# Kernel tuning notes

Measured on AMD Instinct MI355X. Metric: run time of the kernel, lower is better.

## Reference

```python
import jax, jax.numpy as jnp
import numpy as np

S = 30.0   # scale
M = 0.3    # additive angular margin (arcface)
EPS = 1e-07


def setup_inputs() -> dict:
    key = jax.random.key(0)
    k1, k2, k3 = jax.random.split(key, 3)
    N, D, C = 8192, 256, 10000
    x = jax.random.normal(k1, (N, D), dtype=jnp.float32)
    W = jax.random.normal(k2, (C, D), dtype=jnp.float32) * 0.05  # linear weight [C, D]
    target = jax.random.randint(k3, (N,), 0, C)
    return {"x": x, "W": W, "target": target}


def reference(x, W, target):
    # L2-normalize inputs along features. NOTE: the torch code's loop that
    # 'normalizes' weight_fc params is a no-op (rebinds a local), so W is
    # intentionally NOT normalized here, matching the original math.
    xn = x / jnp.linalg.norm(x, axis=1, keepdims=True)
    logits = xn @ W.T                                   # [N, C]
    n = logits.shape[0]
    tgt = logits[jnp.arange(n), target]                 # [N] target-class cosine-like score
    # arcface margin: s * cos(acos(clamp(t)) + m)
    numerator = S * jnp.cos(jnp.arccos(jnp.clip(tgt, -1.0 + EPS, 1.0 - EPS)) + M)
    # exclude-target sum: sum_j exp(s*logits) minus the target column (no [N,C-1] concat)
    exp_s = jnp.exp(S * logits)                         # [N, C]
    sum_excl = jnp.sum(exp_s, axis=1) - jnp.exp(S * tgt)
    denominator = jnp.exp(numerator) + sum_excl
    L = numerator - jnp.log(denominator)
    return -jnp.mean(L)
```

## Files before the change

kernel.cpp:

```cpp
#include <hip/hip_runtime.h>
#include <hip/hip_bf16.h>
#include <stdint.h>

#define S_SCALE 30.0f
#define S_L2E_SC 0.33813165020835f
#define N_ROWS 8192
#define D_DIM 256
#define C_CLS 10000
#define NCB 8

typedef __attribute__((ext_vector_type(4))) float f32x4;

static __device__ __forceinline__ void gl16(const void* g, void* l) {
  __builtin_amdgcn_global_load_lds(
      (const __attribute__((address_space(1))) void*)g,
      (__attribute__((address_space(3))) void*)l, 16, 0, 0);
}

static __device__ __forceinline__ long u2l(uint2 v) {
  union { uint2 u; long l; } x; x.u = v; return x.l;
}

static __device__ __forceinline__ float row_sum16(float v) {
  union { float f; int i; } u, w;
  u.f = v;
  w.i = __builtin_amdgcn_update_dpp(0, u.i, 0xB1, 0xF, 0xF, true);  u.f += w.f;
  w.i = __builtin_amdgcn_update_dpp(0, u.i, 0x4E, 0xF, 0xF, true);  u.f += w.f;
  w.i = __builtin_amdgcn_update_dpp(0, u.i, 0x141, 0xF, 0xF, true); u.f += w.f;
  w.i = __builtin_amdgcn_update_dpp(0, u.i, 0x140, 0xF, 0xF, true); u.f += w.f;
  return u.f;
}

__global__ __launch_bounds__(256) void k_prep(const float* __restrict__ x,
                                              const float* __restrict__ W,
                                              const int* __restrict__ target,
                                              unsigned char* __restrict__ xnb8,
                                              unsigned char* __restrict__ WbF8,
                                              float* __restrict__ tgt) {
  if (blockIdx.x < 1280) {
    int gidx = blockIdx.x * 256 + threadIdx.x;
    int lane = gidx & 63;
    int kc = (gidx >> 6) & 7;
    int c16 = gidx >> 9;
    int col = c16 * 16 + (lane & 15);
    int k0 = kc * 32 + (lane >> 4) * 8;
    int r0 = 0, r1 = 0;
    if (col < C_CLS) {
      const float4 a = *(const float4*)(W + (size_t)col * D_DIM + k0);
      const float4 b = *(const float4*)(W + (size_t)col * D_DIM + k0 + 4);
      r0 = __builtin_amdgcn_cvt_pk_fp8_f32(a.x * 16.f, a.y * 16.f, 0, false);
      r0 = __builtin_amdgcn_cvt_pk_fp8_f32(a.z * 16.f, a.w * 16.f, r0, true);
      r1 = __builtin_amdgcn_cvt_pk_fp8_f32(b.x * 16.f, b.y * 16.f, 0, false);
      r1 = __builtin_amdgcn_cvt_pk_fp8_f32(b.z * 16.f, b.w * 16.f, r1, true);
    }
    *(int2*)(WbF8 + (size_t)gidx * 8) = (int2){r0, r1};
  } else {
    int row = (blockIdx.x - 1280) * 4 + (threadIdx.x >> 6);
    int l = threadIdx.x & 63;
    const float4 v = *(const float4*)(x + (size_t)row * D_DIM + l * 4);
    float ss = v.x * v.x + v.y * v.y + v.z * v.z + v.w * v.w;
#pragma unroll
    for (int m = 1; m < 64; m <<= 1) ss += __shfl_xor(ss, m, 64);
    float rn = 1.0f / sqrtf(ss);
    float s8 = rn * 8.f;
    int r0 = __builtin_amdgcn_cvt_pk_fp8_f32(v.x * s8, v.y * s8, 0, false);
    r0 = __builtin_amdgcn_cvt_pk_fp8_f32(v.z * s8, v.w * s8, r0, true);
    int j = l >> 1, e = l & 1;
    int panel = row >> 7, r16 = (row >> 4) & 7, lr = row & 15;
    size_t dst = (size_t)panel * 32768 + (size_t)(r16 * 8 + (j >> 2)) * 512 +
                 (size_t)((j & 3) * 16 + lr) * 8 + e * 4;
    *(int*)(xnb8 + dst) = r0;
    int tc = target[row];
    const float4 b = *(const float4*)(W + (size_t)tc * D_DIM + l * 4);
    float s = v.x * b.x + v.y * b.y + v.z * b.z + v.w * b.w;
#pragma unroll
    for (int m = 1; m < 64; m <<= 1) s += __shfl_xor(s, m, 64);
    if (l == 0) tgt[row] = s * rn;
  }
}

__global__ __launch_bounds__(512, 4) void k_gemm(const unsigned char* __restrict__ xnb8,
                                                 const unsigned char* __restrict__ WbF8,
                                                 float* __restrict__ partials) {
  __shared__ __align__(16) char lds[34816];
  const int b = blockIdx.x;
  const int cg = b & 7;
  const int br = b >> 3;
  const int bc0 = cg * 5;
  const int t = threadIdx.x;
  const int w = t >> 6, l = t & 63;
  const int wr = w >> 2, wc = w & 3;
  const int lr = l & 15, lk = l >> 4;
  float* rsumAll = (float*)(lds + 32768);

  if (t < 512) rsumAll[t] = 0.f;

  {
    const char* Ag = (const char*)xnb8 + (size_t)br * 32768;
#pragma unroll
    for (int i = 0; i < 4; ++i)
      gl16(Ag + i * 8192 + w * 1024 + l * 16, lds + i * 8192 + w * 1024);
    asm volatile("s_waitcnt vmcnt(0)" ::: "memory");
    __builtin_amdgcn_sched_barrier(0);
    __builtin_amdgcn_s_barrier();
  }

  f32x4 acc[4][4];
#pragma unroll
  for (int m = 0; m < 4; m++)
#pragma unroll
    for (int n = 0; n < 4; n++) acc[m][n] = (f32x4){0.f, 0.f, 0.f, 0.f};

  const char* AwL = lds + (size_t)(wr * 4 * 8) * 512 + (size_t)l * 8;
  const unsigned char* Bw = WbF8 + (size_t)(bc0 * 16 + wc * 4) * 4096 + (size_t)l * 8;
  float* rw = rsumAll + w * 64;

  uint2 b0[4], b1[4];
#pragma unroll
  for (int fn = 0; fn < 4; ++fn) b0[fn] = *(const uint2*)(Bw + fn * 4096);

  for (int tt = 0; tt < 5; ++tt) {
    auto step = [&](int kc, uint2(&cur)[4], uint2(&nxt)[4]) {
      if (kc < 7) {
#pragma unroll
        for (int fn = 0; fn < 4; ++fn)
          nxt[fn] = *(const uint2*)(Bw + fn * 4096 + (kc + 1) * 512);
      } else if (tt < 4) {
#pragma unroll
        for (int fn = 0; fn < 4; ++fn)
          nxt[fn] = *(const uint2*)(Bw + 65536 + fn * 4096);
      }
#pragma unroll
      for (int fm = 0; fm < 4; ++fm) {
        long a = u2l(*(const uint2*)(AwL + (fm * 8 + kc) * 512));
#pragma unroll
        for (int fn = 0; fn < 4; ++fn)
          acc[fm][fn] = __builtin_amdgcn_mfma_f32_16x16x32_fp8_fp8(
              a, u2l(cur[fn]), acc[fm][fn], 0, 0, 0);
      }
    };
    step(0, b0, b1); step(1, b1, b0); step(2, b0, b1); step(3, b1, b0);
    step(4, b0, b1); step(5, b1, b0); step(6, b0, b1); step(7, b1, b0);

    const int bc = bc0 + tt;
#pragma unroll
    for (int m = 0; m < 4; ++m) {
      float rs0 = 0.f, rs1 = 0.f, rs2 = 0.f, rs3 = 0.f;
#pragma unroll
      for (int n = 0; n < 4; ++n) {
        int col = bc * 256 + wc * 64 + n * 16 + lr;
        bool ok = (col < C_CLS);
        rs0 += ok ? __builtin_amdgcn_exp2f(acc[m][n][0] * S_L2E_SC) : 0.f;
        rs1 += ok ? __builtin_amdgcn_exp2f(acc[m][n][1] * S_L2E_SC) : 0.f;
        rs2 += ok ? __builtin_amdgcn_exp2f(acc[m][n][2] * S_L2E_SC) : 0.f;
        rs3 += ok ? __builtin_amdgcn_exp2f(acc[m][n][3] * S_L2E_SC) : 0.f;
        acc[m][n] = (f32x4){0.f, 0.f, 0.f, 0.f};
      }
      rs0 = row_sum16(rs0); rs1 = row_sum16(rs1);
      rs2 = row_sum16(rs2); rs3 = row_sum16(rs3);
      if (lr == 0) {
        int row = m * 16 + lk * 4;
        rw[row + 0] += rs0; rw[row + 1] += rs1;
        rw[row + 2] += rs2; rw[row + 3] += rs3;
      }
    }
    Bw += 65536;
  }

  __syncthreads();
  if (t < 128) {
    int wr2 = t >> 6, r = t & 63;
    float sv = rsumAll[(wr2 * 4 + 0) * 64 + r] + rsumAll[(wr2 * 4 + 1) * 64 + r] +
               rsumAll[(wr2 * 4 + 2) * 64 + r] + rsumAll[(wr2 * 4 + 3) * 64 + r];
    partials[(size_t)cg * N_ROWS + (size_t)br * 128 + t] = sv;
  }
}

__global__ __launch_bounds__(256) void k_loss1(const float* __restrict__ partials,
                                               const float* __restrict__ tgt,
                                               float* __restrict__ bsum) {
  __shared__ float wsum[4];
  int i = blockIdx.x * 256 + threadIdx.x;
  const float* p = partials + i;
  float s = 0.f;
#pragma unroll
  for (int j = 0; j < NCB; ++j) s += p[(size_t)j * N_ROWS];
  float tl = tgt[i];
  float tcv = fminf(fmaxf(tl, -1.0f + 1e-7f), 1.0f - 1e-7f);
  const float cm = 0.95533648912560601964f;
  const float sm = 0.29552020666133957510f;
  float num = S_SCALE * (tcv * cm - sqrtf(fmaxf(1.0f - tcv * tcv, 0.f)) * sm);
  float sum_excl = s - __expf(S_SCALE * tl);
  float denom = __expf(num) + sum_excl;
  float L = num - __logf(denom);
#pragma unroll
  for (int m = 1; m < 64; m <<= 1) L += __shfl_xor(L, m, 64);
  int l = threadIdx.x & 63, w = threadIdx.x >> 6;
  if (l == 0) wsum[w] = L;
  __syncthreads();
  if (threadIdx.x == 0) bsum[blockIdx.x] = wsum[0] + wsum[1] + wsum[2] + wsum[3];
}

__global__ void k_loss2(const float* __restrict__ bsum, float* __restrict__ out) {
  float s = 0.f;
  for (int i = 0; i < 32; ++i) s += bsum[i];
  out[0] = -s / (float)N_ROWS;
}

extern "C" void kernel_launch(void* const* d_in, const int* in_sizes, int n_in,
                              void* d_out, int out_size, void* d_ws, size_t ws_size,
                              hipStream_t stream) {
  const float* x = (const float*)d_in[0];
  const float* W = (const float*)d_in[1];
  const int* target = (const int*)d_in[2];
  float* out = (float*)d_out;
  char* ws = (char*)d_ws;

  unsigned char* xnb8 = (unsigned char*)(ws);
  unsigned char* WbF8 = (unsigned char*)(ws + 2097152);
  float* tgt = (float*)(ws + 4718592);
  float* partials = (float*)(ws + 4751360);
  float* bsum = (float*)(ws + 5013504);

  k_prep<<<3328, 256, 0, stream>>>(x, W, target, xnb8, WbF8, tgt);
  k_gemm<<<512, 512, 0, stream>>>(xnb8, WbF8, partials);
  k_loss1<<<32, 256, 0, stream>>>(partials, tgt, bsum);
  k_loss2<<<1, 1, 0, stream>>>(bsum, out);
}
```

Before: 53.31 us.

## Switch GEMM to 32x32x16 FP8 MFMA tiles and drop padded-column masking

```diff
diff --git a/kernel.cpp b/kernel.cpp
--- a/kernel.cpp
+++ b/kernel.cpp
@@ -9,7 +9,7 @@
 #define C_CLS 10000
 #define NCB 8
 
-typedef __attribute__((ext_vector_type(4))) float f32x4;
+typedef __attribute__((ext_vector_type(16))) float f32x16;
 
 static __device__ __forceinline__ void gl16(const void* g, void* l) {
   __builtin_amdgcn_global_load_lds(
@@ -21,13 +21,14 @@
   union { uint2 u; long l; } x; x.u = v; return x.l;
 }
 
-static __device__ __forceinline__ float row_sum16(float v) {
+static __device__ __forceinline__ float row_sum32(float v) {
   union { float f; int i; } u, w;
   u.f = v;
   w.i = __builtin_amdgcn_update_dpp(0, u.i, 0xB1, 0xF, 0xF, true);  u.f += w.f;
   w.i = __builtin_amdgcn_update_dpp(0, u.i, 0x4E, 0xF, 0xF, true);  u.f += w.f;
   w.i = __builtin_amdgcn_update_dpp(0, u.i, 0x141, 0xF, 0xF, true); u.f += w.f;
   w.i = __builtin_amdgcn_update_dpp(0, u.i, 0x140, 0xF, 0xF, true); u.f += w.f;
+  u.f += __shfl_xor(u.f, 16, 64);
   return u.f;
 }
 
@@ -40,10 +41,10 @@
   if (blockIdx.x < 1280) {
     int gidx = blockIdx.x * 256 + threadIdx.x;
     int lane = gidx & 63;
-    int kc = (gidx >> 6) & 7;
-    int c16 = gidx >> 9;
-    int col = c16 * 16 + (lane & 15);
-    int k0 = kc * 32 + (lane >> 4) * 8;
+    int kc = (gidx >> 6) & 15;
+    int c32 = gidx >> 10;
+    int col = c32 * 32 + (lane & 31);
+    int k0 = kc * 16 + (lane >> 5) * 8;
     int r0 = 0, r1 = 0;
     if (col < C_CLS) {
       const float4 a = *(const float4*)(W + (size_t)col * D_DIM + k0);
@@ -65,10 +66,9 @@
     float s8 = rn * 8.f;
     int r0 = __builtin_amdgcn_cvt_pk_fp8_f32(v.x * s8, v.y * s8, 0, false);
     r0 = __builtin_amdgcn_cvt_pk_fp8_f32(v.z * s8, v.w * s8, r0, true);
-    int j = l >> 1, e = l & 1;
-    int panel = row >> 7, r16 = (row >> 4) & 7, lr = row & 15;
-    size_t dst = (size_t)panel * 32768 + (size_t)(r16 * 8 + (j >> 2)) * 512 +
-                 (size_t)((j & 3) * 16 + lr) * 8 + e * 4;
+    int panel = row >> 7, r32 = (row >> 5) & 3;
+    size_t dst = (size_t)panel * 32768 + (size_t)(r32 * 16 + (l >> 2)) * 512 +
+                 (size_t)((row & 31) + 32 * ((l >> 1) & 1)) * 8 + (l & 1) * 4;
     *(int*)(xnb8 + dst) = r0;
     int tc = target[row];
     const float4 b = *(const float4*)(W + (size_t)tc * D_DIM + l * 4);
@@ -90,7 +90,6 @@
   const int t = threadIdx.x;
   const int w = t >> 6, l = t & 63;
   const int wr = w >> 2, wc = w & 3;
-  const int lr = l & 15, lk = l >> 4;
   float* rsumAll = (float*)(lds + 32768);
 
   if (t < 512) rsumAll[t] = 0.f;
@@ -105,63 +104,60 @@
     __builtin_amdgcn_s_barrier();
   }
 
-  f32x4 acc[4][4];
-#pragma unroll
-  for (int m = 0; m < 4; m++)
-#pragma unroll
-    for (int n = 0; n < 4; n++) acc[m][n] = (f32x4){0.f, 0.f, 0.f, 0.f};
-
-  const char* AwL = lds + (size_t)(wr * 4 * 8) * 512 + (size_t)l * 8;
-  const unsigned char* Bw = WbF8 + (size_t)(bc0 * 16 + wc * 4) * 4096 + (size_t)l * 8;
+  f32x16 acc[2][2];
+#pragma unroll
+  for (int m = 0; m < 2; m++)
+#pragma unroll
+    for (int n = 0; n < 2; n++)
+#pragma unroll
+      for (int j = 0; j < 16; j++) acc[m][n][j] = 0.f;
+
+  const char* AwL = lds + (size_t)wr * 16384 + (size_t)l * 8;
+  const unsigned char* Bw = WbF8 + (size_t)(bc0 * 8 + wc * 2) * 8192 + (size_t)l * 8;
   float* rw = rsumAll + w * 64;
 
-  uint2 b0[4], b1[4];
-#pragma unroll
-  for (int fn = 0; fn < 4; ++fn) b0[fn] = *(const uint2*)(Bw + fn * 4096);
+  uint2 b0[2], b1[2];
+#pragma unroll
+  for (int fn = 0; fn < 2; ++fn) b0[fn] = *(const uint2*)(Bw + fn * 8192);
 
   for (int tt = 0; tt < 5; ++tt) {
-    auto step = [&](int kc, uint2(&cur)[4], uint2(&nxt)[4]) {
-      if (kc < 7) {
-#pragma unroll
-        for (int fn = 0; fn < 4; ++fn)
-          nxt[fn] = *(const uint2*)(Bw + fn * 4096 + (kc + 1) * 512);
+    auto step = [&](int kc, uint2(&cur)[2], uint2(&nxt)[2]) {
+      if (kc < 15) {
+#pragma unroll
+        for (int fn = 0; fn < 2; ++fn)
+          nxt[fn] = *(const uint2*)(Bw + fn * 8192 + (kc + 1) * 512);
       } else if (tt < 4) {
 #pragma unroll
-        for (int fn = 0; fn < 4; ++fn)
-          nxt[fn] = *(const uint2*)(Bw + 65536 + fn * 4096);
+        for (int fn = 0; fn < 2; ++fn)
+          nxt[fn] = *(const uint2*)(Bw + 65536 + fn * 8192);
       }
 #pragma unroll
-      for (int fm = 0; fm < 4; ++fm) {
-        long a = u2l(*(const uint2*)(AwL + (fm * 8 + kc) * 512));
-#pragma unroll
-        for (int fn = 0; fn < 4; ++fn)
-          acc[fm][fn] = __builtin_amdgcn_mfma_f32_16x16x32_fp8_fp8(
+      for (int fm = 0; fm < 2; ++fm) {
+        long a = u2l(*(const uint2*)(AwL + (fm * 16 + kc) * 512));
+#pragma unroll
+        for (int fn = 0; fn < 2; ++fn)
+          acc[fm][fn] = __builtin_amdgcn_mfma_f32_32x32x16_fp8_fp8(
               a, u2l(cur[fn]), acc[fm][fn], 0, 0, 0);
       }
     };
-    step(0, b0, b1); step(1, b1, b0); step(2, b0, b1); step(3, b1, b0);
-    step(4, b0, b1); step(5, b1, b0); step(6, b0, b1); step(7, b1, b0);
-
-    const int bc = bc0 + tt;
-#pragma unroll
-    for (int m = 0; m < 4; ++m) {
-      float rs0 = 0.f, rs1 = 0.f, rs2 = 0.f, rs3 = 0.f;
-#pragma unroll
-      for (int n = 0; n < 4; ++n) {
-        int col = bc * 256 + wc * 64 + n * 16 + lr;
-        bool ok = (col < C_CLS);
-        rs0 += ok ? __builtin_amdgcn_exp2f(acc[m][n][0] * S_L2E_SC) : 0.f;
-        rs1 += ok ? __builtin_amdgcn_exp2f(acc[m][n][1] * S_L2E_SC) : 0.f;
-        rs2 += ok ? __builtin_amdgcn_exp2f(acc[m][n][2] * S_L2E_SC) : 0.f;
-        rs3 += ok ? __builtin_amdgcn_exp2f(acc[m][n][3] * S_L2E_SC) : 0.f;
-        acc[m][n] = (f32x4){0.f, 0.f, 0.f, 0.f};
-      }
-      rs0 = row_sum16(rs0); rs1 = row_sum16(rs1);
-      rs2 = row_sum16(rs2); rs3 = row_sum16(rs3);
-      if (lr == 0) {
-        int row = m * 16 + lk * 4;
-        rw[row + 0] += rs0; rw[row + 1] += rs1;
-        rw[row + 2] += rs2; rw[row + 3] += rs3;
+    step(0, b0, b1);  step(1, b1, b0);  step(2, b0, b1);  step(3, b1, b0);
+    step(4, b0, b1);  step(5, b1, b0);  step(6, b0, b1);  step(7, b1, b0);
+    step(8, b0, b1);  step(9, b1, b0);  step(10, b0, b1); step(11, b1, b0);
+    step(12, b0, b1); step(13, b1, b0); step(14, b0, b1); step(15, b1, b0);
+
+#pragma unroll
+    for (int fm = 0; fm < 2; ++fm) {
+#pragma unroll
+      for (int j = 0; j < 16; ++j) {
+        float rs = __builtin_amdgcn_exp2f(acc[fm][0][j] * S_L2E_SC) +
+                   __builtin_amdgcn_exp2f(acc[fm][1][j] * S_L2E_SC);
+        rs = row_sum32(rs);
+        if ((l & 31) == 0) {
+          int row = fm * 32 + (j & 3) + 8 * (j >> 2) + 4 * (l >> 5);
+          rw[row] += rs;
+        }
+        acc[fm][0][j] = 0.f;
+        acc[fm][1][j] = 0.f;
       }
     }
     Bw += 65536;
@@ -182,7 +178,7 @@
   __shared__ float wsum[4];
   int i = blockIdx.x * 256 + threadIdx.x;
   const float* p = partials + i;
-  float s = 0.f;
+  float s = -240.0f;
 #pragma unroll
   for (int j = 0; j < NCB; ++j) s += p[(size_t)j * N_ROWS];
   float tl = tgt[i];
```

After: 57.17 us. 1.07x slower.

## Shrink GEMM tiles to 64x128 blocks of 256 threads and drop column masking

Applied to the files above, without the earlier changes.

```diff
diff --git a/kernel.cpp b/kernel.cpp
--- a/kernel.cpp
+++ b/kernel.cpp
@@ -7,7 +7,7 @@
 #define N_ROWS 8192
 #define D_DIM 256
 #define C_CLS 10000
-#define NCB 8
+#define NCB 16
 
 typedef __attribute__((ext_vector_type(4))) float f32x4;
 
@@ -65,10 +65,9 @@
     float s8 = rn * 8.f;
     int r0 = __builtin_amdgcn_cvt_pk_fp8_f32(v.x * s8, v.y * s8, 0, false);
     r0 = __builtin_amdgcn_cvt_pk_fp8_f32(v.z * s8, v.w * s8, r0, true);
-    int j = l >> 1, e = l & 1;
-    int panel = row >> 7, r16 = (row >> 4) & 7, lr = row & 15;
-    size_t dst = (size_t)panel * 32768 + (size_t)(r16 * 8 + (j >> 2)) * 512 +
-                 (size_t)((j & 3) * 16 + lr) * 8 + e * 4;
+    int panel = row >> 6, r16 = (row >> 4) & 3, lr = row & 15;
+    size_t dst = (size_t)panel * 16384 + (size_t)(r16 * 8 + (l >> 3)) * 512 +
+                 (size_t)(((l >> 1) & 3) * 16 + lr) * 8 + (l & 1) * 4;
     *(int*)(xnb8 + dst) = r0;
     int tc = target[row];
     const float4 b = *(const float4*)(W + (size_t)tc * D_DIM + l * 4);
@@ -79,83 +78,82 @@
   }
 }
 
-__global__ __launch_bounds__(512, 4) void k_gemm(const unsigned char* __restrict__ xnb8,
+__global__ __launch_bounds__(256, 5) void k_gemm(const unsigned char* __restrict__ xnb8,
                                                  const unsigned char* __restrict__ WbF8,
                                                  float* __restrict__ partials) {
-  __shared__ __align__(16) char lds[34816];
+  __shared__ __align__(16) char lds[17408];
   const int b = blockIdx.x;
   const int cg = b & 7;
-  const int br = b >> 3;
-  const int bc0 = cg * 5;
+  const int sub = (b >> 3) & 1;
+  const int rp = b >> 4;
   const int t = threadIdx.x;
   const int w = t >> 6, l = t & 63;
-  const int wr = w >> 2, wc = w & 3;
   const int lr = l & 15, lk = l >> 4;
-  float* rsumAll = (float*)(lds + 32768);
-
-  if (t < 512) rsumAll[t] = 0.f;
+  float* rsumAll = (float*)(lds + 16384);
+
+  rsumAll[t] = 0.f;
 
   {
-    const char* Ag = (const char*)xnb8 + (size_t)br * 32768;
+    const char* Ag = (const char*)xnb8 + (size_t)rp * 16384;
 #pragma unroll
     for (int i = 0; i < 4; ++i)
-      gl16(Ag + i * 8192 + w * 1024 + l * 16, lds + i * 8192 + w * 1024);
+      gl16(Ag + i * 4096 + t * 16, lds + i * 4096 + w * 1024);
     asm volatile("s_waitcnt vmcnt(0)" ::: "memory");
     __builtin_amdgcn_sched_barrier(0);
     __builtin_amdgcn_s_barrier();
   }
 
-  f32x4 acc[4][4];
+  f32x4 acc[4][2];
 #pragma unroll
   for (int m = 0; m < 4; m++)
 #pragma unroll
-    for (int n = 0; n < 4; n++) acc[m][n] = (f32x4){0.f, 0.f, 0.f, 0.f};
-
-  const char* AwL = lds + (size_t)(wr * 4 * 8) * 512 + (size_t)l * 8;
-  const unsigned char* Bw = WbF8 + (size_t)(bc0 * 16 + wc * 4) * 4096 + (size_t)l * 8;
+    for (int n = 0; n < 2; n++) acc[m][n] = (f32x4){0.f, 0.f, 0.f, 0.f};
+
+  const char* AwL = lds + (size_t)l * 8;
+  const unsigned char* Bw = WbF8 + ((size_t)(cg * 2 + sub) * 40 + w * 2) * 4096 +
+                            (size_t)l * 8;
   float* rw = rsumAll + w * 64;
 
-  uint2 b0[4], b1[4];
-#pragma unroll
-  for (int fn = 0; fn < 4; ++fn) b0[fn] = *(const uint2*)(Bw + fn * 4096);
+  uint2 b0[2], b1[2];
+  b0[0] = *(const uint2*)(Bw);
+  b0[1] = *(const uint2*)(Bw + 4096);
 
   for (int tt = 0; tt < 5; ++tt) {
-    auto step = [&](int kc, uint2(&cur)[4], uint2(&nxt)[4]) {
+    auto step = [&](int kc, uint2(&cur)[2], uint2(&nxt)[2]) {
       if (kc < 7) {
-#pragma unroll
-        for (int fn = 0; fn < 4; ++fn)
-          nxt[fn] = *(const uint2*)(Bw + fn * 4096 + (kc + 1) * 512);
+        nxt[0] = *(const uint2*)(Bw + (kc + 1) * 512);
+        nxt[1] = *(const uint2*)(Bw + 4096 + (kc + 1) * 512);
       } else if (tt < 4) {
-#pragma unroll
-        for (int fn = 0; fn < 4; ++fn)
-          nxt[fn] = *(const uint2*)(Bw + 65536 + fn * 4096);
+        nxt[0] = *(const uint2*)(Bw + 32768);
+        nxt[1] = *(const uint2*)(Bw + 32768 + 4096);
       }
+      __builtin_amdgcn_s_setprio(1);
 #pragma unroll
       for (int fm = 0; fm < 4; ++fm) {
         long a = u2l(*(const uint2*)(AwL + (fm * 8 + kc) * 512));
-#pragma unroll
-        for (int fn = 0; fn < 4; ++fn)
-          acc[fm][fn] = __builtin_amdgcn_mfma_f32_16x16x32_fp8_fp8(
-              a, u2l(cur[fn]), acc[fm][fn], 0, 0, 0);
+        acc[fm][0] = __builtin_amdgcn_mfma_f32_16x16x32_fp8_fp8(
+            a, u2l(cur[0]), acc[fm][0], 0, 0, 0);
+        acc[fm][1] = __builtin_amdgcn_mfma_f32_16x16x32_fp8_fp8(
+            a, u2l(cur[1]), acc[fm][1], 0, 0, 0);
       }
+      __builtin_amdgcn_s_setprio(0);
     };
     step(0, b0, b1); step(1, b1, b0); step(2, b0, b1); step(3, b1, b0);
     step(4, b0, b1); step(5, b1, b0); step(6, b0, b1); step(7, b1, b0);
 
-    const int bc = bc0 + tt;
 #pragma unroll
     for (int m = 0; m < 4; ++m) {
-      float rs0 = 0.f, rs1 = 0.f, rs2 = 0.f, rs3 = 0.f;
-#pragma unroll
-      for (int n = 0; n < 4; ++n) {
-        int col = bc * 256 + wc * 64 + n * 16 + lr;
-        bool ok = (col < C_CLS);
-        rs0 += ok ? __builtin_amdgcn_exp2f(acc[m][n][0] * S_L2E_SC) : 0.f;
-        rs1 += ok ? __builtin_amdgcn_exp2f(acc[m][n][1] * S_L2E_SC) : 0.f;
-        rs2 += ok ? __builtin_amdgcn_exp2f(acc[m][n][2] * S_L2E_SC) : 0.f;
-        rs3 += ok ? __builtin_amdgcn_exp2f(acc[m][n][3] * S_L2E_SC) : 0.f;
-        acc[m][n] = (f32x4){0.f, 0.f, 0.f, 0.f};
-      }
+      float rs0, rs1, rs2, rs3;
+      rs0 = __builtin_amdgcn_exp2f(acc[m][0][0] * S_L2E_SC) +
+            __builtin_amdgcn_exp2f(acc[m][1][0] * S_L2E_SC);
+      rs1 = __builtin_amdgcn_exp2f(acc[m][0][1] * S_L2E_SC) +
+            __builtin_amdgcn_exp2f(acc[m][1][1] * S_L2E_SC);
+      rs2 = __builtin_amdgcn_exp2f(acc[m][0][2] * S_L2E_SC) +
+            __builtin_amdgcn_exp2f(acc[m][1][2] * S_L2E_SC);
+      rs3 = __builtin_amdgcn_exp2f(acc[m][0][3] * S_L2E_SC) +
+            __builtin_amdgcn_exp2f(acc[m][1][3] * S_L2E_SC);
+      acc[m][0] = (f32x4){0.f, 0.f, 0.f, 0.f};
+      acc[m][1] = (f32x4){0.f, 0.f, 0.f, 0.f};
       rs0 = row_sum16(rs0); rs1 = row_sum16(rs1);
       rs2 = row_sum16(rs2); rs3 = row_sum16(rs3);
       if (lr == 0) {
@@ -164,15 +162,13 @@
         rw[row + 2] += rs2; rw[row + 3] += rs3;
       }
     }
-    Bw += 65536;
+    Bw += 32768;
   }
 
   __syncthreads();
-  if (t < 128) {
-    int wr2 = t >> 6, r = t & 63;
-    float sv = rsumAll[(wr2 * 4 + 0) * 64 + r] + rsumAll[(wr2 * 4 + 1) * 64 + r] +
-               rsumAll[(wr2 * 4 + 2) * 64 + r] + rsumAll[(wr2 * 4 + 3) * 64 + r];
-    partials[(size_t)cg * N_ROWS + (size_t)br * 128 + t] = sv;
+  if (t < 64) {
+    float sv = rsumAll[t] + rsumAll[64 + t] + rsumAll[128 + t] + rsumAll[192 + t];
+    partials[(size_t)(cg * 2 + sub) * N_ROWS + (size_t)rp * 64 + t] = sv;
   }
 }
 
@@ -182,7 +178,7 @@
   __shared__ float wsum[4];
   int i = blockIdx.x * 256 + threadIdx.x;
   const float* p = partials + i;
-  float s = 0.f;
+  float s = -240.0f;
 #pragma unroll
   for (int j = 0; j < NCB; ++j) s += p[(size_t)j * N_ROWS];
   float tl = tgt[i];
@@ -220,10 +216,10 @@
   unsigned char* WbF8 = (unsigned char*)(ws + 2097152);
   float* tgt = (float*)(ws + 4718592);
   float* partials = (float*)(ws + 4751360);
-  float* bsum = (float*)(ws + 5013504);
+  float* bsum = (float*)(ws + 5275648);
 
   k_prep<<<3328, 256, 0, stream>>>(x, W, target, xnb8, WbF8, tgt);
-  k_gemm<<<512, 512, 0, stream>>>(xnb8, WbF8, partials);
+  k_gemm<<<2048, 256, 0, stream>>>(xnb8, WbF8, partials);
   k_loss1<<<32, 256, 0, stream>>>(partials, tgt, bsum);
   k_loss2<<<1, 1, 0, stream>>>(bsum, out);
 }
```

Result: slower. 87.79 us (+64.7%).
